# Kernel optimization log

Measured on AMD Instinct MI355X. Metric: run time of the kernel, lower is better.

Reference implementation:

```python
import jax, jax.numpy as jnp
import numpy as np

N, F, C, E = 1024, 64, 4, 32768
H = 256       # MLP hidden width
C_OUT = 4     # new edge channels produced by nn_edge


def setup_inputs() -> dict:
    key = jax.random.key(0)
    ks = jax.random.split(key, 12)
    x = jax.random.normal(ks[0], (N, F), dtype=jnp.float32)
    edge_index = jax.random.randint(ks[1], (C, 2, E), 0, N)
    edge_weight = jax.random.uniform(ks[2], (C, E), dtype=jnp.float32)
    s_n1 = 1.0 / np.sqrt(C * F)
    s_n2 = 1.0 / np.sqrt(H)
    s_e1 = 1.0 / np.sqrt(C + 2 * F)
    return {
        "x": x,
        "edge_index": edge_index,
        "edge_weight": edge_weight,
        "Wn1": jax.random.normal(ks[3], (C * F, H), dtype=jnp.float32) * s_n1,
        "bn1": jnp.zeros((H,), jnp.float32),
        "Wn2": jax.random.normal(ks[4], (H, F), dtype=jnp.float32) * s_n2,
        "bn2": jnp.zeros((F,), jnp.float32),
        "We1": jax.random.normal(ks[5], (C + 2 * F, H), dtype=jnp.float32) * s_e1,
        "be1": jnp.zeros((H,), jnp.float32),
        "We2": jax.random.normal(ks[6], (H, C_OUT), dtype=jnp.float32) * s_n2,
        "be2": jnp.zeros((C_OUT,), jnp.float32),
        "eps": jnp.zeros((), jnp.float32),
    }


def reference(x, edge_index, edge_weight, Wn1, bn1, Wn2, bn2, We1, be1, We2, be2, eps):
    # ---- MCGNN: per-channel edge-weighted scatter-add aggregation ----
    def agg_one(ei, w):
        # ei: [2,E] (row0 = source j, row1 = target i); w: [E]
        msg = x[ei[0]] * w[:, None]                       # [E,F]
        return jax.ops.segment_sum(msg, ei[1], num_segments=N)  # [N,F]

    agg = jax.vmap(agg_one)(edge_index, edge_weight)      # [C,N,F]
    out_cat = agg + (1.0 + eps) * x                       # broadcast self term
    h = out_cat.transpose(1, 0, 2).reshape(N, C * F)      # [N, C*F]
    x_next = jax.nn.relu(h @ Wn1 + bn1) @ Wn2 + bn2       # [N,F]

    # ---- EDPGNN: dense adjacency per channel + broadcast x_i/x_j ----
    def dense_adj(ei, w):
        return jnp.zeros((N, N), x.dtype).at[ei[0], ei[1]].add(w)

    a = jax.vmap(dense_adj)(edge_index, edge_weight)      # [C,N,N]
    a = a.transpose(1, 2, 0)                              # [N,N,C]
    x_i = jnp.broadcast_to(x_next[:, None, :], (N, N, F))
    x_j = jnp.broadcast_to(x_next[None, :, :], (N, N, F))
    feat = jnp.concatenate([a, x_i, x_j], axis=2).reshape(N * N, C + 2 * F)
    adj_out = (jax.nn.relu(feat @ We1 + be1) @ We2 + be2).reshape(N, N, C_OUT)
    return adj_out
```

## Files before the change

### kernel.cpp

```cpp
#include <hip/hip_runtime.h>

#define NN 1024
#define FF 64
#define CC 4
#define EE 32768
#define HH 256

#define OFF_PART  0u
#define OFF_OFFS  65536u
#define OFF_SRT   66564u
#define OFF_P     328708u
#define OFF_Q     590852u

__global__ __launch_bounds__(1024)
void k_hist(const int* __restrict__ ei, int* __restrict__ partial)
{
    __shared__ int h[1024];
    const int tid = threadIdx.x, blk = blockIdx.x;
    h[tid] = 0;
    __syncthreads();
#pragma unroll
    for (int u = 0; u < 2; ++u) {
        int t = blk * 2048 + u * 1024 + tid;
        int e = t & (EE - 1), c = t >> 15;
        int src = ei[c * 2 * EE + e];
        int dst = ei[c * 2 * EE + EE + e];
        atomicAdd(&h[(src >> 5) * 32 + (dst >> 5)], 1);
    }
    __syncthreads();
    partial[blk * 1024 + tid] = h[tid];
}

__global__ __launch_bounds__(1024)
void k_offsets(int* __restrict__ partial, int* __restrict__ offs)
{
    __shared__ int wsum[16];
    const int b = threadIdx.x;
    int run = 0;
    for (int blk = 0; blk < 64; ++blk) {
        int v = partial[blk * 1024 + b];
        partial[blk * 1024 + b] = run;
        run += v;
    }
    int incl = run;
#pragma unroll
    for (int d = 1; d < 64; d <<= 1) {
        int v = __shfl_up(incl, d, 64);
        if ((b & 63) >= d) incl += v;
    }
    const int w = b >> 6;
    if ((b & 63) == 63) wsum[w] = incl;
    __syncthreads();
    int base = incl - run;
    for (int ww = 0; ww < w; ++ww) base += wsum[ww];
    offs[b] = base;
    if (b == 1023) offs[1024] = base + run;
    for (int blk = 0; blk < 64; ++blk) partial[blk * 1024 + b] += base;
}

__global__ __launch_bounds__(1024)
void k_scatter(const int* __restrict__ ei, const float* __restrict__ ew,
               const int* __restrict__ partial, int2* __restrict__ srt)
{
    __shared__ int cnt[1024];
    const int tid = threadIdx.x, blk = blockIdx.x;
    cnt[tid] = 0;
    __syncthreads();
#pragma unroll
    for (int u = 0; u < 2; ++u) {
        int t = blk * 2048 + u * 1024 + tid;
        int e = t & (EE - 1), c = t >> 15;
        int src = ei[c * 2 * EE + e];
        int dst = ei[c * 2 * EE + EE + e];
        float w = ew[c * EE + e];
        int bkt = (src >> 5) * 32 + (dst >> 5);
        int r = atomicAdd(&cnt[bkt], 1);
        srt[partial[blk * 1024 + bkt] + r] =
            make_int2(((src & 31) << 7) | ((dst & 31) << 2) | c, __float_as_int(w));
    }
}

__global__ __launch_bounds__(1024)
void k_node(const float* __restrict__ x, const int* __restrict__ ei,
            const float* __restrict__ ew,
            const float* __restrict__ Wn1, const float* __restrict__ bn1,
            const float* __restrict__ Wn2, const float* __restrict__ bn2,
            const float* __restrict__ We1, const float* __restrict__ be1,
            const float* __restrict__ epsp,
            float* __restrict__ P, float* __restrict__ Q)
{
    __shared__ float hval[4][256];
    __shared__ float hidl[4][256];
    __shared__ float part[4][4][64];
    __shared__ float xnl[4][64];
    __shared__ int2 list[1024];
    __shared__ int nM;
    const int tid = threadIdx.x;
    const int n0 = blockIdx.x * 4;

    ((float*)hval)[tid] = 0.f;
    if (tid == 0) nM = 0;
    __syncthreads();

    for (int u = 0; u < 32; ++u) {
        int t4 = u * 4096 + tid * 4;
        int e = t4 & (EE - 1), c = t4 >> 15;
        int4 d4 = *(const int4*)(ei + c * 2 * EE + EE + e);
        unsigned m0 = (unsigned)(d4.x - n0), m1 = (unsigned)(d4.y - n0);
        unsigned m2 = (unsigned)(d4.z - n0), m3 = (unsigned)(d4.w - n0);
        if ((m0 < 4u) | (m1 < 4u) | (m2 < 4u) | (m3 < 4u)) {
            unsigned mm[4] = {m0, m1, m2, m3};
#pragma unroll
            for (int k = 0; k < 4; ++k) {
                if (mm[k] < 4u) {
                    int src = ei[c * 2 * EE + e + k];
                    float w = ew[c * EE + e + k];
                    int idx = atomicAdd(&nM, 1);
                    list[idx] = make_int2((mm[k] << 12) | (c << 10) | src, __float_as_int(w));
                }
            }
        }
    }
    __syncthreads();

    {
        const int wv = tid >> 6, lane = tid & 63;
        const int n = nM;
        for (int idx = wv; idx < n; idx += 16) {
            int2 e2 = list[idx];
            int nn = (e2.x >> 12) & 3, c = (e2.x >> 10) & 3, src = e2.x & 1023;
            atomicAdd(&hval[nn][c * 64 + lane],
                      __int_as_float(e2.y) * x[src * FF + lane]);
        }
    }
    __syncthreads();

    {
        const float ope = 1.0f + epsp[0];
        const int nn = tid >> 8;
        ((float*)hval)[tid] += ope * x[(n0 + nn) * FF + (tid & 63)];
    }
    __syncthreads();

    {
        const int nn = tid >> 8, h = tid & 255;
        float acc = bn1[h];
#pragma unroll 8
        for (int k = 0; k < 256; ++k)
            acc += hval[nn][k] * Wn1[k * 256 + h];
        hidl[nn][h] = fmaxf(acc, 0.f);
    }
    __syncthreads();

    {
        const int kq = tid >> 8, nn = (tid >> 6) & 3, f = tid & 63;
        float p = 0.f;
#pragma unroll 8
        for (int k = kq * 64; k < kq * 64 + 64; ++k)
            p += hidl[nn][k] * Wn2[k * 64 + f];
        part[kq][nn][f] = p;
    }
    __syncthreads();
    if (tid < 256) {
        const int nn = tid >> 6, f = tid & 63;
        xnl[nn][f] = bn2[f] + part[0][nn][f] + part[1][nn][f]
                             + part[2][nn][f] + part[3][nn][f];
    }
    __syncthreads();

    {
        const int r = tid >> 8, h = tid & 255;
        float p = be1[h], q = 0.f;
#pragma unroll 8
        for (int f = 0; f < 64; ++f) {
            float xv = xnl[r][f];
            p += xv * We1[(4 + f) * 256 + h];
            q += xv * We1[(68 + f) * 256 + h];
        }
        P[(n0 + r) * 256 + h] = p;
        Q[(n0 + r) * 256 + h] = q;
    }
}

__global__ __launch_bounds__(256, 4)
void k_edge_mlp(const float* __restrict__ P, const float* __restrict__ Q,
                const int* __restrict__ toffs, const int2* __restrict__ srt,
                const float* __restrict__ We1, const float* __restrict__ We2,
                const float* __restrict__ be2, float* __restrict__ out)
{
    __shared__ float4 aT[32 * 32];
    __shared__ float4 PQbuf[1024];
    __shared__ unsigned short list[1024];
    __shared__ int nList;

    const int tid = threadIdx.x;
    const int bi = blockIdx.y, bj = blockIdx.x;
    const int iBase = bi * 32, jBase = bj * 32;

#pragma unroll
    for (int u = 0; u < 4; ++u)
        aT[tid + u * 256] = make_float4(0.f, 0.f, 0.f, 0.f);
    if (tid == 0) nList = 0;
    __syncthreads();

    {
        const int tile = bi * 32 + bj;
        const int beg = toffs[tile], end = toffs[tile + 1];
        float* aTf = (float*)aT;
        for (int k = beg + tid; k < end; k += 256) {
            int2 e2 = srt[k];
            int li = (e2.x >> 7) & 31, lj = (e2.x >> 2) & 31, c = e2.x & 3;
            atomicAdd(&aTf[(li * 32 + lj) * 4 + c], __int_as_float(e2.y));
        }
    }
    __syncthreads();

#pragma unroll
    for (int u = 0; u < 4; ++u) {
        int p = tid * 4 + u;
        float4 a4 = aT[p];
        if (a4.x != 0.f || a4.y != 0.f || a4.z != 0.f || a4.w != 0.f) {
            int idx = atomicAdd(&nList, 1);
            list[idx] = (unsigned short)p;
        }
    }
    __syncthreads();
    const int nL = nList;

    int myp[4];
    float4 mya[4], mycc[4];
#pragma unroll
    for (int k = 0; k < 4; ++k) {
        int en = tid + k * 256;
        if (en < nL) { myp[k] = list[en]; mya[k] = aT[myp[k]]; }
        else         { myp[k] = -1; mya[k] = make_float4(0.f, 0.f, 0.f, 0.f); }
        mycc[k] = make_float4(0.f, 0.f, 0.f, 0.f);
    }

    const int tx = tid & 15, ty = tid >> 4;
    const int psw = ty & 7, qsw = tx & 7;

    float4 acc[2][2];
#pragma unroll
    for (int ii = 0; ii < 2; ++ii)
#pragma unroll
        for (int jj = 0; jj < 2; ++jj)
            acc[ii][jj] = make_float4(0.f, 0.f, 0.f, 0.f);

    for (int hc = 0; hc < 4; ++hc) {
#pragma unroll
        for (int u = 0; u < 2; ++u) {
            int idx = tid + u * 256;
            int row = idx >> 4, q = idx & 15;
            int ph = q ^ ((row >> 1) & 7);
            PQbuf[row * 16 + ph]       = *(const float4*)(P + (iBase + row) * 256 + hc * 64 + q * 4);
            PQbuf[512 + row * 16 + ph] = *(const float4*)(Q + (jBase + row) * 256 + hc * 64 + q * 4);
        }
        __syncthreads();

#pragma unroll 4
        for (int q = 0; q < 16; ++q) {
            float4 w2[4];
#pragma unroll
            for (int k = 0; k < 4; ++k)
                w2[k] = *(const float4*)(We2 + (hc * 64 + q * 4 + k) * 4);
            float4 p[2], qv[2];
#pragma unroll
            for (int r = 0; r < 2; ++r) p[r]  = PQbuf[(ty * 2 + r) * 16 + (q ^ psw)];
#pragma unroll
            for (int r = 0; r < 2; ++r) qv[r] = PQbuf[512 + (tx * 2 + r) * 16 + (q ^ qsw)];
#pragma unroll
            for (int ii = 0; ii < 2; ++ii) {
#pragma unroll
                for (int jj = 0; jj < 2; ++jj) {
                    float v0 = fmaxf(p[ii].x + qv[jj].x, 0.f);
                    float v1 = fmaxf(p[ii].y + qv[jj].y, 0.f);
                    float v2 = fmaxf(p[ii].z + qv[jj].z, 0.f);
                    float v3 = fmaxf(p[ii].w + qv[jj].w, 0.f);
                    acc[ii][jj].x += v0 * w2[0].x + v1 * w2[1].x + v2 * w2[2].x + v3 * w2[3].x;
                    acc[ii][jj].y += v0 * w2[0].y + v1 * w2[1].y + v2 * w2[2].y + v3 * w2[3].y;
                    acc[ii][jj].z += v0 * w2[0].z + v1 * w2[1].z + v2 * w2[2].z + v3 * w2[3].z;
                    acc[ii][jj].w += v0 * w2[0].w + v1 * w2[1].w + v2 * w2[2].w + v3 * w2[3].w;
                }
            }
        }

#pragma unroll
        for (int k = 0; k < 4; ++k) {
            if (myp[k] < 0) continue;
            const int li = myp[k] >> 5, lj = myp[k] & 31;
            const int ps2 = (li >> 1) & 7, qs2 = (lj >> 1) & 7;
            const float4 a4 = mya[k];
            float4 cc = mycc[k];
#pragma unroll 4
            for (int q = 0; q < 16; ++q) {
                float4 w1[4], w2[4];
#pragma unroll
                for (int c = 0; c < 4; ++c)
                    w1[c] = *(const float4*)(We1 + c * 256 + hc * 64 + q * 4);
#pragma unroll
                for (int kk = 0; kk < 4; ++kk)
                    w2[kk] = *(const float4*)(We2 + (hc * 64 + q * 4 + kk) * 4);
                float4 pv = PQbuf[li * 16 + (q ^ ps2)];
                float4 qv = PQbuf[512 + lj * 16 + (q ^ qs2)];
                float s0 = a4.x * w1[0].x + a4.y * w1[1].x + a4.z * w1[2].x + a4.w * w1[3].x;
                float s1 = a4.x * w1[0].y + a4.y * w1[1].y + a4.z * w1[2].y + a4.w * w1[3].y;
                float s2 = a4.x * w1[0].z + a4.y * w1[1].z + a4.z * w1[2].z + a4.w * w1[3].z;
                float s3 = a4.x * w1[0].w + a4.y * w1[1].w + a4.z * w1[2].w + a4.w * w1[3].w;
                float b0 = pv.x + qv.x, b1 = pv.y + qv.y, b2_ = pv.z + qv.z, b3 = pv.w + qv.w;
                float d0 = fmaxf(b0 + s0, 0.f) - fmaxf(b0, 0.f);
                float d1 = fmaxf(b1 + s1, 0.f) - fmaxf(b1, 0.f);
                float d2 = fmaxf(b2_ + s2, 0.f) - fmaxf(b2_, 0.f);
                float d3 = fmaxf(b3 + s3, 0.f) - fmaxf(b3, 0.f);
                cc.x += d0 * w2[0].x + d1 * w2[1].x + d2 * w2[2].x + d3 * w2[3].x;
                cc.y += d0 * w2[0].y + d1 * w2[1].y + d2 * w2[2].y + d3 * w2[3].y;
                cc.z += d0 * w2[0].z + d1 * w2[1].z + d2 * w2[2].z + d3 * w2[3].z;
                cc.w += d0 * w2[0].w + d1 * w2[1].w + d2 * w2[2].w + d3 * w2[3].w;
            }
            mycc[k] = cc;
        }
        __syncthreads();
    }

    float4* corr = PQbuf;
#pragma unroll
    for (int u = 0; u < 4; ++u)
        corr[tid + u * 256] = make_float4(0.f, 0.f, 0.f, 0.f);
    __syncthreads();
#pragma unroll
    for (int k = 0; k < 4; ++k)
        if (myp[k] >= 0) corr[myp[k]] = mycc[k];
    __syncthreads();

    const float4 b2 = *(const float4*)be2;
#pragma unroll
    for (int ii = 0; ii < 2; ++ii)
#pragma unroll
        for (int jj = 0; jj < 2; ++jj) {
            int p = (ty * 2 + ii) * 32 + (tx * 2 + jj);
            float4 cr = corr[p];
            float4 o = acc[ii][jj];
            o.x += b2.x + cr.x; o.y += b2.y + cr.y;
            o.z += b2.z + cr.z; o.w += b2.w + cr.w;
            *(float4*)(out + ((size_t)(iBase + ty * 2 + ii) * NN + (jBase + tx * 2 + jj)) * 4) = o;
        }
}

extern "C" void kernel_launch(void* const* d_in, const int* in_sizes, int n_in,
                              void* d_out, int out_size, void* d_ws, size_t ws_size,
                              hipStream_t stream)
{
    (void)in_sizes; (void)n_in; (void)out_size; (void)ws_size;
    const float* x   = (const float*)d_in[0];
    const int*   ei  = (const int*)d_in[1];
    const float* ew  = (const float*)d_in[2];
    const float* Wn1 = (const float*)d_in[3];
    const float* bn1 = (const float*)d_in[4];
    const float* Wn2 = (const float*)d_in[5];
    const float* bn2 = (const float*)d_in[6];
    const float* We1 = (const float*)d_in[7];
    const float* be1 = (const float*)d_in[8];
    const float* We2 = (const float*)d_in[9];
    const float* be2 = (const float*)d_in[10];
    const float* eps = (const float*)d_in[11];
    float* out = (float*)d_out;

    float* ws = (float*)d_ws;
    int*  partial = (int*)(ws + OFF_PART);
    int*  offs    = (int*)(ws + OFF_OFFS);
    int2* srt     = (int2*)(ws + OFF_SRT);
    float* Pb     = ws + OFF_P;
    float* Qb     = ws + OFF_Q;

    k_hist   <<<64, 1024, 0, stream>>>(ei, partial);
    k_offsets<<<1, 1024, 0, stream>>>(partial, offs);
    k_scatter<<<64, 1024, 0, stream>>>(ei, ew, partial, srt);
    k_node   <<<NN / 4, 1024, 0, stream>>>(x, ei, ew, Wn1, bn1, Wn2, bn2,
                                           We1, be1, eps, Pb, Qb);

    dim3 g(NN / 32, NN / 32);
    k_edge_mlp<<<g, 256, 0, stream>>>(Pb, Qb, offs, srt, We1, We2, be2, out);
}
```

Baseline: 250.4 us.

## Reuse tile-sorted edge list in node kernel and alias edge-MLP shared buffers

The node kernel now builds its incoming-edge list from the tile-bucketed sorted edge array, reading only the 32 tiles in its destination column instead of scanning all edges for every block. The histogram and scatter kernels use 128 blocks of one edge per thread, and the partial-count array is transposed so the offsets kernel reads each bucket's counts contiguously. The edge-MLP kernel reuses one shared buffer for the adjacency tile and the P/Q staging, which lets the occupancy hint rise from 4 to 6 blocks per SM, at the cost of one extra barrier.

```diff
diff --git a/kernel.cpp b/kernel.cpp
--- a/kernel.cpp
+++ b/kernel.cpp
@@ -7,10 +7,10 @@
 #define HH 256
 
 #define OFF_PART  0u
-#define OFF_OFFS  65536u
-#define OFF_SRT   66564u
-#define OFF_P     328708u
-#define OFF_Q     590852u
+#define OFF_OFFS  131072u
+#define OFF_SRT   132100u
+#define OFF_P     394244u
+#define OFF_Q     656388u
 
 __global__ __launch_bounds__(1024)
 void k_hist(const int* __restrict__ ei, int* __restrict__ partial)
@@ -19,16 +19,13 @@
     const int tid = threadIdx.x, blk = blockIdx.x;
     h[tid] = 0;
     __syncthreads();
-#pragma unroll
-    for (int u = 0; u < 2; ++u) {
-        int t = blk * 2048 + u * 1024 + tid;
-        int e = t & (EE - 1), c = t >> 15;
-        int src = ei[c * 2 * EE + e];
-        int dst = ei[c * 2 * EE + EE + e];
-        atomicAdd(&h[(src >> 5) * 32 + (dst >> 5)], 1);
-    }
-    __syncthreads();
-    partial[blk * 1024 + tid] = h[tid];
+    int t = blk * 1024 + tid;
+    int e = t & (EE - 1), c = t >> 15;
+    int src = ei[c * 2 * EE + e];
+    int dst = ei[c * 2 * EE + EE + e];
+    atomicAdd(&h[(src >> 5) * 32 + (dst >> 5)], 1);
+    __syncthreads();
+    partial[tid * 128 + blk] = h[tid];
 }
 
 __global__ __launch_bounds__(1024)
@@ -37,9 +34,9 @@
     __shared__ int wsum[16];
     const int b = threadIdx.x;
     int run = 0;
-    for (int blk = 0; blk < 64; ++blk) {
-        int v = partial[blk * 1024 + b];
-        partial[blk * 1024 + b] = run;
+    for (int blk = 0; blk < 128; ++blk) {
+        int v = partial[b * 128 + blk];
+        partial[b * 128 + blk] = run;
         run += v;
     }
     int incl = run;
@@ -55,7 +52,7 @@
     for (int ww = 0; ww < w; ++ww) base += wsum[ww];
     offs[b] = base;
     if (b == 1023) offs[1024] = base + run;
-    for (int blk = 0; blk < 64; ++blk) partial[blk * 1024 + b] += base;
+    for (int blk = 0; blk < 128; ++blk) partial[b * 128 + blk] += base;
 }
 
 __global__ __launch_bounds__(1024)
@@ -66,23 +63,20 @@
     const int tid = threadIdx.x, blk = blockIdx.x;
     cnt[tid] = 0;
     __syncthreads();
-#pragma unroll
-    for (int u = 0; u < 2; ++u) {
-        int t = blk * 2048 + u * 1024 + tid;
-        int e = t & (EE - 1), c = t >> 15;
-        int src = ei[c * 2 * EE + e];
-        int dst = ei[c * 2 * EE + EE + e];
-        float w = ew[c * EE + e];
-        int bkt = (src >> 5) * 32 + (dst >> 5);
-        int r = atomicAdd(&cnt[bkt], 1);
-        srt[partial[blk * 1024 + bkt] + r] =
-            make_int2(((src & 31) << 7) | ((dst & 31) << 2) | c, __float_as_int(w));
-    }
+    int t = blk * 1024 + tid;
+    int e = t & (EE - 1), c = t >> 15;
+    int src = ei[c * 2 * EE + e];
+    int dst = ei[c * 2 * EE + EE + e];
+    float w = ew[c * EE + e];
+    int bkt = (src >> 5) * 32 + (dst >> 5);
+    int r = atomicAdd(&cnt[bkt], 1);
+    srt[partial[bkt * 128 + blk] + r] =
+        make_int2(((src & 31) << 7) | ((dst & 31) << 2) | c, __float_as_int(w));
 }
 
 __global__ __launch_bounds__(1024)
-void k_node(const float* __restrict__ x, const int* __restrict__ ei,
-            const float* __restrict__ ew,
+void k_node(const float* __restrict__ x, const int* __restrict__ toffs,
+            const int2* __restrict__ srt,
             const float* __restrict__ Wn1, const float* __restrict__ bn1,
             const float* __restrict__ Wn2, const float* __restrict__ bn2,
             const float* __restrict__ We1, const float* __restrict__ be1,
@@ -97,26 +91,26 @@
     __shared__ int nM;
     const int tid = threadIdx.x;
     const int n0 = blockIdx.x * 4;
+    const int jt = n0 >> 5;
+    const int w0 = n0 & 31;
 
     ((float*)hval)[tid] = 0.f;
     if (tid == 0) nM = 0;
     __syncthreads();
 
-    for (int u = 0; u < 32; ++u) {
-        int t4 = u * 4096 + tid * 4;
-        int e = t4 & (EE - 1), c = t4 >> 15;
-        int4 d4 = *(const int4*)(ei + c * 2 * EE + EE + e);
-        unsigned m0 = (unsigned)(d4.x - n0), m1 = (unsigned)(d4.y - n0);
-        unsigned m2 = (unsigned)(d4.z - n0), m3 = (unsigned)(d4.w - n0);
-        if ((m0 < 4u) | (m1 < 4u) | (m2 < 4u) | (m3 < 4u)) {
-            unsigned mm[4] = {m0, m1, m2, m3};
-#pragma unroll
-            for (int k = 0; k < 4; ++k) {
-                if (mm[k] < 4u) {
-                    int src = ei[c * 2 * EE + e + k];
-                    float w = ew[c * EE + e + k];
+    {
+        const int wv = tid >> 6, lane = tid & 63;
+        for (int i = wv; i < 32; i += 16) {
+            const int tile = i * 32 + jt;
+            const int beg = toffs[tile], end = toffs[tile + 1];
+            for (int k = beg + lane; k < end; k += 64) {
+                int2 e2 = srt[k];
+                unsigned m = (unsigned)(((e2.x >> 2) & 31) - w0);
+                if (m < 4u) {
+                    int src = i * 32 + ((e2.x >> 7) & 31);
+                    int c = e2.x & 3;
                     int idx = atomicAdd(&nM, 1);
-                    list[idx] = make_int2((mm[k] << 12) | (c << 10) | src, __float_as_int(w));
+                    list[idx] = make_int2((m << 12) | (c << 10) | src, e2.y);
                 }
             }
         }
@@ -182,14 +176,13 @@
     }
 }
 
-__global__ __launch_bounds__(256, 4)
+__global__ __launch_bounds__(256, 6)
 void k_edge_mlp(const float* __restrict__ P, const float* __restrict__ Q,
                 const int* __restrict__ toffs, const int2* __restrict__ srt,
                 const float* __restrict__ We1, const float* __restrict__ We2,
                 const float* __restrict__ be2, float* __restrict__ out)
 {
-    __shared__ float4 aT[32 * 32];
-    __shared__ float4 PQbuf[1024];
+    __shared__ float4 buf[1024];
     __shared__ unsigned short list[1024];
     __shared__ int nList;
 
@@ -199,14 +192,14 @@
 
 #pragma unroll
     for (int u = 0; u < 4; ++u)
-        aT[tid + u * 256] = make_float4(0.f, 0.f, 0.f, 0.f);
+        buf[tid + u * 256] = make_float4(0.f, 0.f, 0.f, 0.f);
     if (tid == 0) nList = 0;
     __syncthreads();
 
     {
         const int tile = bi * 32 + bj;
         const int beg = toffs[tile], end = toffs[tile + 1];
-        float* aTf = (float*)aT;
+        float* aTf = (float*)buf;
         for (int k = beg + tid; k < end; k += 256) {
             int2 e2 = srt[k];
             int li = (e2.x >> 7) & 31, lj = (e2.x >> 2) & 31, c = e2.x & 3;
@@ -218,7 +211,7 @@
 #pragma unroll
     for (int u = 0; u < 4; ++u) {
         int p = tid * 4 + u;
-        float4 a4 = aT[p];
+        float4 a4 = buf[p];
         if (a4.x != 0.f || a4.y != 0.f || a4.z != 0.f || a4.w != 0.f) {
             int idx = atomicAdd(&nList, 1);
             list[idx] = (unsigned short)p;
@@ -232,10 +225,11 @@
 #pragma unroll
     for (int k = 0; k < 4; ++k) {
         int en = tid + k * 256;
-        if (en < nL) { myp[k] = list[en]; mya[k] = aT[myp[k]]; }
+        if (en < nL) { myp[k] = list[en]; mya[k] = buf[myp[k]]; }
         else         { myp[k] = -1; mya[k] = make_float4(0.f, 0.f, 0.f, 0.f); }
         mycc[k] = make_float4(0.f, 0.f, 0.f, 0.f);
     }
+    __syncthreads();
 
     const int tx = tid & 15, ty = tid >> 4;
     const int psw = ty & 7, qsw = tx & 7;
@@ -253,8 +247,8 @@
             int idx = tid + u * 256;
             int row = idx >> 4, q = idx & 15;
             int ph = q ^ ((row >> 1) & 7);
-            PQbuf[row * 16 + ph]       = *(const float4*)(P + (iBase + row) * 256 + hc * 64 + q * 4);
-            PQbuf[512 + row * 16 + ph] = *(const float4*)(Q + (jBase + row) * 256 + hc * 64 + q * 4);
+            buf[row * 16 + ph]       = *(const float4*)(P + (iBase + row) * 256 + hc * 64 + q * 4);
+            buf[512 + row * 16 + ph] = *(const float4*)(Q + (jBase + row) * 256 + hc * 64 + q * 4);
         }
         __syncthreads();
 
@@ -266,9 +260,9 @@
                 w2[k] = *(const float4*)(We2 + (hc * 64 + q * 4 + k) * 4);
             float4 p[2], qv[2];
 #pragma unroll
-            for (int r = 0; r < 2; ++r) p[r]  = PQbuf[(ty * 2 + r) * 16 + (q ^ psw)];
-#pragma unroll
-            for (int r = 0; r < 2; ++r) qv[r] = PQbuf[512 + (tx * 2 + r) * 16 + (q ^ qsw)];
+            for (int r = 0; r < 2; ++r) p[r]  = buf[(ty * 2 + r) * 16 + (q ^ psw)];
+#pragma unroll
+            for (int r = 0; r < 2; ++r) qv[r] = buf[512 + (tx * 2 + r) * 16 + (q ^ qsw)];
 #pragma unroll
             for (int ii = 0; ii < 2; ++ii) {
 #pragma unroll
@@ -301,8 +295,8 @@
 #pragma unroll
                 for (int kk = 0; kk < 4; ++kk)
                     w2[kk] = *(const float4*)(We2 + (hc * 64 + q * 4 + kk) * 4);
-                float4 pv = PQbuf[li * 16 + (q ^ ps2)];
-                float4 qv = PQbuf[512 + lj * 16 + (q ^ qs2)];
+                float4 pv = buf[li * 16 + (q ^ ps2)];
+                float4 qv = buf[512 + lj * 16 + (q ^ qs2)];
                 float s0 = a4.x * w1[0].x + a4.y * w1[1].x + a4.z * w1[2].x + a4.w * w1[3].x;
                 float s1 = a4.x * w1[0].y + a4.y * w1[1].y + a4.z * w1[2].y + a4.w * w1[3].y;
                 float s2 = a4.x * w1[0].z + a4.y * w1[1].z + a4.z * w1[2].z + a4.w * w1[3].z;
@@ -322,14 +316,13 @@
         __syncthreads();
     }
 
-    float4* corr = PQbuf;
 #pragma unroll
     for (int u = 0; u < 4; ++u)
-        corr[tid + u * 256] = make_float4(0.f, 0.f, 0.f, 0.f);
+        buf[tid + u * 256] = make_float4(0.f, 0.f, 0.f, 0.f);
     __syncthreads();
 #pragma unroll
     for (int k = 0; k < 4; ++k)
-        if (myp[k] >= 0) corr[myp[k]] = mycc[k];
+        if (myp[k] >= 0) buf[myp[k]] = mycc[k];
     __syncthreads();
 
     const float4 b2 = *(const float4*)be2;
@@ -338,7 +331,7 @@
 #pragma unroll
         for (int jj = 0; jj < 2; ++jj) {
             int p = (ty * 2 + ii) * 32 + (tx * 2 + jj);
-            float4 cr = corr[p];
+            float4 cr = buf[p];
             float4 o = acc[ii][jj];
             o.x += b2.x + cr.x; o.y += b2.y + cr.y;
             o.z += b2.z + cr.z; o.w += b2.w + cr.w;
@@ -372,10 +365,10 @@
     float* Pb     = ws + OFF_P;
     float* Qb     = ws + OFF_Q;
 
-    k_hist   <<<64, 1024, 0, stream>>>(ei, partial);
+    k_hist   <<<128, 1024, 0, stream>>>(ei, partial);
     k_offsets<<<1, 1024, 0, stream>>>(partial, offs);
-    k_scatter<<<64, 1024, 0, stream>>>(ei, ew, partial, srt);
-    k_node   <<<NN / 4, 1024, 0, stream>>>(x, ei, ew, Wn1, bn1, Wn2, bn2,
+    k_scatter<<<128, 1024, 0, stream>>>(ei, ew, partial, srt);
+    k_node   <<<NN / 4, 1024, 0, stream>>>(x, offs, srt, Wn1, bn1, Wn2, bn2,
                                            We1, be1, eps, Pb, Qb);
 
     dim3 g(NN / 32, NN / 32);
```

Result: slower. 311.7 us (+24.4%).
